# Performance work log

Measured on AMD Instinct MI355X. Metric: run time of the kernel, lower is better.

## Reference

```python
import jax, jax.numpy as jnp
import numpy as np

H = 128          # GRU hidden size (fixed in module)
EPS = 1e-8       # torch CosineSimilarity eps


def _gru_dir(x, w_ih, w_hh, b_ih, b_hh, reverse):
    # x: [B, L, D]; torch GRU gate math, single direction
    B = x.shape[0]
    gx = jnp.einsum('bld,gd->blg', x, w_ih) + b_ih  # [B, L, 3H]

    def step(h, gx_t):
        gh = h @ w_hh.T + b_hh
        xr, xz, xn = jnp.split(gx_t, 3, axis=-1)
        hr, hz, hn = jnp.split(gh, 3, axis=-1)
        r = jax.nn.sigmoid(xr + hr)
        z = jax.nn.sigmoid(xz + hz)
        n = jnp.tanh(xn + r * hn)
        h_new = (1.0 - z) * n + z * h
        return h_new, h_new

    h0 = jnp.zeros((B, H), x.dtype)
    h_last, outs = jax.lax.scan(step, h0, jnp.swapaxes(gx, 0, 1), reverse=reverse)
    return jnp.swapaxes(outs, 0, 1), h_last  # [B, L, H], [B, H]


def _bigru(x, p):
    # p = (w_ih_f, w_hh_f, b_ih_f, b_hh_f, w_ih_b, w_hh_b, b_ih_b, b_hh_b)
    of, hf = _gru_dir(x, p[0], p[1], p[2], p[3], False)
    ob, hb = _gru_dir(x, p[4], p[5], p[6], p[7], True)
    # outs concat = torch bidirectional output; [hf, hb] concat == h_n.transpose(1,0).reshape(B,-1)
    return jnp.concatenate([of, ob], axis=-1), jnp.concatenate([hf, hb], axis=-1)


def _cosnorm(x):
    return x / jnp.maximum(jnp.linalg.norm(x, axis=-1, keepdims=True), EPS)


def _forward(context, options, rnn_p, attn_p):
    ctx_outs, ctx_h = _bigru(context, rnn_p)  # [B, L1, 2H], [B, 2H]

    def per_option(option):  # option: [B, L2, D]
        opt_outs, _ = _bigru(option, rnn_p)  # [B, L2, 2H]
        # cosine-similarity attention == matmul of L2-normalized vectors
        # (replaces the original O(B*L2*L1*2H) repeated tensors, same math)
        att = jnp.einsum('bqh,bkh->bqk', _cosnorm(opt_outs), _cosnorm(ctx_outs))  # [B, L2, L1]
        att = jax.nn.softmax(att, axis=2)  # softmax over context positions (dim=2)
        att_opt = jnp.einsum('bqk,bkh->bqh', att, ctx_outs)  # bmm -> [B, L2, 2H]
        cat = jnp.concatenate([att_opt, opt_outs], axis=-1)  # [B, L2, 4H]
        _, ao_h = _bigru(cat, attn_p)  # [B, 2H]
        num = jnp.sum(ctx_h * ao_h, axis=-1)
        den = jnp.maximum(jnp.linalg.norm(ctx_h, axis=-1), EPS) * \
              jnp.maximum(jnp.linalg.norm(ao_h, axis=-1), EPS)
        return num / den  # [B]

    logits = jax.vmap(per_option)(jnp.swapaxes(options, 0, 1))  # [N, B]
    return jax.nn.softmax(logits.T, axis=1)  # [B, N]


def setup_inputs():
    key = jax.random.key(0)
    ks = jax.random.split(key, 24)
    B, L1, L2, N, D = 64, 512, 50, 10, 300
    inp = {
        'context': jax.random.normal(ks[0], (B, L1, D), jnp.float32),
        'context_lens': jax.random.randint(ks[1], (B,), 1, L1),
        'options': jax.random.normal(ks[2], (B, N, L2, D), jnp.float32),
        'option_lens': jax.random.randint(ks[3], (B, N), 1, L2),
    }
    names = ['rw_ih_f', 'rw_hh_f', 'rb_ih_f', 'rb_hh_f',
             'rw_ih_b', 'rw_hh_b', 'rb_ih_b', 'rb_hh_b',
             'aw_ih_f', 'aw_hh_f', 'ab_ih_f', 'ab_hh_f',
             'aw_ih_b', 'aw_hh_b', 'ab_ih_b', 'ab_hh_b']
    shapes = [(3 * H, D), (3 * H, H), (3 * H,), (3 * H,)] * 2 + \
             [(3 * H, 4 * H), (3 * H, H), (3 * H,), (3 * H,)] * 2
    for i, (n, sh) in enumerate(zip(names, shapes)):
        inp[n] = jax.random.normal(ks[4 + i], sh, jnp.float32) * 0.05
    return inp


def reference(context, context_lens, options, option_lens,
              rw_ih_f, rw_hh_f, rb_ih_f, rb_hh_f,
              rw_ih_b, rw_hh_b, rb_ih_b, rb_hh_b,
              aw_ih_f, aw_hh_f, ab_ih_f, ab_hh_f,
              aw_ih_b, aw_hh_b, ab_ih_b, ab_hh_b):
    rnn_p = (rw_ih_f, rw_hh_f, rb_ih_f, rb_hh_f, rw_ih_b, rw_hh_b, rb_ih_b, rb_hh_b)
    attn_p = (aw_ih_f, aw_hh_f, ab_ih_f, ab_hh_f, aw_ih_b, aw_hh_b, ab_ih_b, ab_hh_b)
    return _forward(context, options, rnn_p, attn_p)
```

## Files before the change

kernel.cpp:

```cpp
#include <hip/hip_runtime.h>
#include <math.h>

#define EPS 1e-8f

typedef _Float16 h2_t __attribute__((ext_vector_type(2)));
typedef _Float16 half8 __attribute__((ext_vector_type(8)));
typedef float f32x4 __attribute__((ext_vector_type(4)));

__device__ __forceinline__ float fsig(float x)  { return 1.0f / (1.0f + __expf(-x)); }
__device__ __forceinline__ float ftanh(float x) { return 1.0f - 2.0f / (1.0f + __expf(2.0f * x)); }

__device__ __forceinline__ void gload16(const _Float16* g, _Float16* lds) {
    __builtin_amdgcn_global_load_lds(
        (const __attribute__((address_space(1))) void*)g,
        (__attribute__((address_space(3))) void*)lds, 16, 0, 0);
}

__device__ __forceinline__ float qsum4(float x) {
    int y1 = __builtin_amdgcn_update_dpp(
        0, __builtin_bit_cast(int, x), 0xB1, 0xF, 0xF, true);
    float s1 = x + __builtin_bit_cast(float, y1);
    int y2 = __builtin_amdgcn_update_dpp(
        0, __builtin_bit_cast(int, s1), 0x4E, 0xF, 0xF, true);
    return s1 + __builtin_bit_cast(float, y2);
}

__global__ __launch_bounds__(256) void prep_w_k(
    const float* __restrict__ rwf, const float* __restrict__ rwb,
    const float* __restrict__ awf, const float* __restrict__ awb,
    const float* __restrict__ rbf, const float* __restrict__ rbb,
    const float* __restrict__ abf, const float* __restrict__ abb,
    const float* __restrict__ rhf, const float* __restrict__ rhb,
    const float* __restrict__ ahf, const float* __restrict__ ahb,
    _Float16* __restrict__ wrh, _Float16* __restrict__ wah,
    _Float16* __restrict__ wr16, _Float16* __restrict__ wa16,
    float* __restrict__ br, float* __restrict__ ba)
{
    int idx = blockIdx.x * 256 + threadIdx.x;
    if (idx < 768 * 320) {
        int g = idx / 320, k = idx % 320;
        float v = 0.f;
        if (k < 300) v = (g < 384) ? rwf[g * 300 + k] : rwb[(g - 384) * 300 + k];
        wrh[idx] = (_Float16)v;
    }
    if (idx < 768 * 512) {
        int g = idx / 512, k = idx % 512;
        wah[idx] = (_Float16)((g < 384) ? awf[g * 512 + k] : awb[(g - 384) * 512 + k]);
    }
    if (idx < 2 * 384 * 128) {
        int d = idx / 49152, r = idx % 49152;
        wr16[idx] = (_Float16)(d ? rhb[r] : rhf[r]);
        wa16[idx] = (_Float16)(d ? ahb[r] : ahf[r]);
    }
    if (idx < 768) {
        br[idx] = (idx < 384) ? rbf[idx] : rbb[idx - 384];
        ba[idx] = (idx < 384) ? abf[idx] : abb[idx - 384];
    }
}

__global__ __launch_bounds__(256) void conv_k(
    const float* __restrict__ ctx, const float* __restrict__ opt,
    _Float16* __restrict__ ctxh, _Float16* __restrict__ opth)
{
    int idx = blockIdx.x * 256 + threadIdx.x;
    if (idx < 32768 * 320) {
        int r = idx / 320, k = idx % 320;
        ctxh[idx] = (k < 300) ? (_Float16)ctx[r * 300 + k] : (_Float16)0.f;
    }
    if (idx < 32000 * 320) {
        int r = idx / 320, k = idx % 320;
        opth[idx] = (k < 300) ? (_Float16)opt[r * 300 + k] : (_Float16)0.f;
    }
}

template <bool TRBS, bool SPLITA, bool HASBIAS, bool DIRECT>
__global__ __launch_bounds__(256, 4) void hgemm_k(
    const _Float16* __restrict__ A, const _Float16* __restrict__ A2,
    const _Float16* __restrict__ B, const float* __restrict__ bias,
    _Float16* __restrict__ C, int M, int N, int K,
    int lda, int ldb, int ldc, long sA, long sB, int bdiv, long sC)
{
    static_assert(!(DIRECT && TRBS), "DIRECT requires NT B layout");
    const int jn = blockIdx.x * 64;
    const int im = blockIdx.y * 64;
    const int z  = blockIdx.z;
    const _Float16* Bb = B + (size_t)(z / bdiv) * sB;
    _Float16* Cb = C + (size_t)z * sC;

    __shared__ __align__(16) _Float16 As[64 * 64];
    __shared__ __align__(16) _Float16 Bs[64 * 64];

    const int tid  = threadIdx.x;
    const int arow = tid >> 2;
    const int akof = (tid & 3) * 8;
    const int lane = tid & 63;
    const int wv   = tid >> 6;
    const int wm   = (wv & 1) * 32;
    const int wn   = (wv >> 1) * 32;
    const int fm   = lane & 15;
    const int quad = lane >> 4;

    f32x4 acc[2][2];
#pragma unroll
    for (int a = 0; a < 2; a++)
#pragma unroll
        for (int b = 0; b < 2; b++) acc[a][b] = (f32x4)0.f;

    for (int k0 = 0; k0 < K; k0 += 64) {
        if constexpr (DIRECT) {
            const int r8 = lane >> 3;
            const int kg = k0 + (lane & 7) * 8;
#pragma unroll
            for (int hh = 0; hh < 2; hh++) {
                const int rb = 8 * (wv + 4 * hh);
                const _Float16* gA;
                if constexpr (SPLITA) {
                    const _Float16* Ah  = A  + (size_t)z * sA;
                    const _Float16* A2h = A2 + (size_t)z * sA;
                    gA = (kg < 256)
                        ? (Ah  + (size_t)(im + rb + r8) * lda + kg)
                        : (A2h + (size_t)(im + rb + r8) * lda + (kg - 256));
                } else {
                    gA = A + (size_t)z * sA + (size_t)(im + rb + r8) * lda + kg;
                }
                gload16(gA, &As[rb * 64]);
                gload16(Bb + (size_t)(jn + rb + r8) * ldb + kg, &Bs[rb * 64]);
            }
        } else {
            {
                const int row = im + arow;
#pragma unroll
                for (int hh = 0; hh < 2; hh++) {
                    half8 av = (half8)(_Float16)0.f;
                    const int kg = k0 + akof + 32 * hh;
                    if (row < M) {
                        if constexpr (SPLITA) {
                            const _Float16* Ah  = A + (size_t)z * sA;
                            const _Float16* A2h = A2 + (size_t)z * sA;
                            const _Float16* ap = (kg < 256)
                                ? (Ah + (size_t)row * lda + kg)
                                : (A2h + (size_t)row * lda + (kg - 256));
                            av = *(const half8*)ap;
                        } else {
                            av = *(const half8*)(A + (size_t)z * sA + (size_t)row * lda + kg);
                        }
                    }
                    *(half8*)&As[arow * 64 + akof + 32 * hh] = av;
                }
            }
            if constexpr (!TRBS) {
#pragma unroll
                for (int hh = 0; hh < 2; hh++) {
                    half8 bv = *(const half8*)(Bb + (size_t)(jn + arow) * ldb
                                               + k0 + akof + 32 * hh);
                    *(half8*)&Bs[arow * 64 + akof + 32 * hh] = bv;
                }
            } else {
                const int kk = tid >> 3, noff = (tid & 7) * 8;
                half8 bv0 = *(const half8*)(Bb + (size_t)(k0 + kk) * ldb + jn + noff);
                half8 bv1 = *(const half8*)(Bb + (size_t)(k0 + kk + 32) * ldb + jn + noff);
#pragma unroll
                for (int e = 0; e < 8; e++) {
                    Bs[(noff + e) * 64 + kk]      = bv0[e];
                    Bs[(noff + e) * 64 + kk + 32] = bv1[e];
                }
            }
        }
        __syncthreads();

        const _Float16* Asp = As + (wm + fm) * 64 + quad * 8;
        const _Float16* Bsp = Bs + (wn + fm) * 64 + quad * 8;
#pragma unroll
        for (int kh = 0; kh < 64; kh += 32) {
            half8 a0 = *(const half8*)(Asp + kh);
            half8 a1 = *(const half8*)(Asp + 16 * 64 + kh);
            half8 b0 = *(const half8*)(Bsp + kh);
            half8 b1 = *(const half8*)(Bsp + 16 * 64 + kh);
            acc[0][0] = __builtin_amdgcn_mfma_f32_16x16x32_f16(a0, b0, acc[0][0], 0, 0, 0);
            acc[0][1] = __builtin_amdgcn_mfma_f32_16x16x32_f16(a0, b1, acc[0][1], 0, 0, 0);
            acc[1][0] = __builtin_amdgcn_mfma_f32_16x16x32_f16(a1, b0, acc[1][0], 0, 0, 0);
            acc[1][1] = __builtin_amdgcn_mfma_f32_16x16x32_f16(a1, b1, acc[1][1], 0, 0, 0);
        }
        __syncthreads();
    }

#pragma unroll
    for (int tm = 0; tm < 2; tm++) {
#pragma unroll
        for (int tn = 0; tn < 2; tn++) {
            const int col  = jn + wn + tn * 16 + fm;
            const int row0 = im + wm + tm * 16 + quad * 4;
            const float bv = HASBIAS ? bias[col] : 0.f;
#pragma unroll
            for (int r = 0; r < 4; r++) {
                const int row = row0 + r;
                if (DIRECT || row < M)
                    Cb[(size_t)row * ldc + col] = (_Float16)(acc[tm][tn][r] + bv);
            }
        }
    }
}

template <int TCMAX>
__global__ __launch_bounds__(512, 2) void gru_rec_k(
    const _Float16* __restrict__ gx,
    const _Float16* __restrict__ whh16,
    const float* __restrict__ bhh_f, const float* __restrict__ bhh_b,
    _Float16* __restrict__ outs_h, float* __restrict__ hfin, int L)
{
    const int dir = blockIdx.x & 1;
    const int s   = blockIdx.x >> 1;
    const int t   = threadIdx.x;
    const int w   = t >> 6;
    const int l   = t & 63;
    const int i   = w * 16 + (l >> 2);
    const int kq  = l & 3;
    const _Float16* Wd = whh16 + (size_t)dir * 49152;
    const float* bh = dir ? bhh_b : bhh_f;

    h2_t w2[3][16];
#pragma unroll
    for (int j = 0; j < 3; j++) {
        const _Float16* Wr = Wd + (size_t)(i + 128 * j) * 128 + 32 * kq;
#pragma unroll
        for (int q = 0; q < 16; q++)
            w2[j][q] = *(const h2_t*)(Wr + 2 * q);
    }
    const float b0 = bh[i], b1 = bh[i + 128], b2 = bh[i + 256];

    __shared__ __align__(16) _Float16 h1[2][128];
    __shared__ __align__(16) _Float16 gxs[TCMAX][384];
    __shared__ __align__(16) _Float16 outb[TCMAX][128];
    if (t < 128) h1[0][t] = (_Float16)0.f;
    float hprev = 0.f;

    constexpr int NST = (TCMAX * 48 + 511) / 512;
    constexpr int NFL = (TCMAX * 16 + 511) / 512;

    for (int t0 = 0; t0 < L; t0 += TCMAX) {
        const int Tc = (L - t0 < TCMAX) ? (L - t0) : TCMAX;
#pragma unroll
        for (int r = 0; r < NST; r++) {
            const int q = t + 512 * r;
            if (q < Tc * 48) {
                const int j = q / 48, off = (q % 48) * 8;
                const int tt = dir ? (L - 1 - (t0 + j)) : (t0 + j);
                *(half8*)&gxs[j][off] =
                    *(const half8*)(gx + ((size_t)s * L + tt) * 768 + dir * 384 + off);
            }
        }
        __syncthreads();

        for (int j = 0; j < Tc; j++) {
            const int cb = (t0 + j) & 1;
            const float xc0 = (float)gxs[j][i];
            const float xc1 = (float)gxs[j][i + 128];
            const float xc2 = (float)gxs[j][i + 256];
            const h2_t* hp = (const h2_t*)&h1[cb][32 * kq];
            float a0 = 0.f, a1 = 0.f, a2 = 0.f;
#pragma unroll
            for (int q = 0; q < 16; q++) {
                h2_t hq = hp[q];
                a0 = __builtin_amdgcn_fdot2(w2[0][q], hq, a0, false);
                a1 = __builtin_amdgcn_fdot2(w2[1][q], hq, a1, false);
                a2 = __builtin_amdgcn_fdot2(w2[2][q], hq, a2, false);
            }
            a0 = qsum4(a0);
            a1 = qsum4(a1);
            a2 = qsum4(a2);
            const float r  = fsig(xc0 + a0 + b0);
            const float zz = fsig(xc1 + a1 + b1);
            const float n  = ftanh(xc2 + r * (a2 + b2));
            const float hnew = (1.0f - zz) * n + zz * hprev;
            hprev = hnew;
            if (kq == 0) {
                h1[cb ^ 1][i] = (_Float16)hnew;
                outb[j][i]    = (_Float16)hnew;
            }
            __syncthreads();
        }

        if (outs_h) {
#pragma unroll
            for (int r = 0; r < NFL; r++) {
                const int q = t + 512 * r;
                if (q < Tc * 16) {
                    const int j = q / 16, off = (q % 16) * 8;
                    const int tt = dir ? (L - 1 - (t0 + j)) : (t0 + j);
                    *(half8*)(outs_h + ((size_t)s * L + tt) * 256 + dir * 128 + off) =
                        *(const half8*)&outb[j][off];
                }
            }
        }
    }
    if (hfin && kq == 0) hfin[(size_t)s * 256 + dir * 128 + i] = hprev;
}

__global__ __launch_bounds__(256) void rowinv_k(const _Float16* __restrict__ x,
                                                float* __restrict__ rinv)
{
    const int row = blockIdx.x;
    float v = (float)x[(size_t)row * 256 + threadIdx.x];
    float ss = v * v;
#pragma unroll
    for (int o = 32; o > 0; o >>= 1) ss += __shfl_down(ss, o);
    __shared__ float ps[4];
    if ((threadIdx.x & 63) == 0) ps[threadIdx.x >> 6] = ss;
    __syncthreads();
    if (threadIdx.x == 0)
        rinv[row] = 1.0f / fmaxf(sqrtf(ps[0] + ps[1] + ps[2] + ps[3]), EPS);
}

__global__ __launch_bounds__(256) void att_softmax_k(
    _Float16* __restrict__ att, const float* __restrict__ rinv_opt_l,
    const float* __restrict__ rinv_ctx, int sbase)
{
    const int row = blockIdx.x;
    const int b = (sbase + row / 50) / 10;
    _Float16* p = att + (size_t)row * 512;
    const float* rc = rinv_ctx + b * 512;
    const float sA = rinv_opt_l[row];
    const int t = threadIdx.x;

    float v0 = (float)p[t]       * (sA * rc[t]);
    float v1 = (float)p[t + 256] * (sA * rc[t + 256]);

    __shared__ float red[4];
    float m = fmaxf(v0, v1);
#pragma unroll
    for (int o = 32; o > 0; o >>= 1) m = fmaxf(m, __shfl_down(m, o));
    if ((t & 63) == 0) red[t >> 6] = m;
    __syncthreads();
    m = fmaxf(fmaxf(red[0], red[1]), fmaxf(red[2], red[3]));
    float e0 = __expf(v0 - m), e1 = __expf(v1 - m);
    float ssum = e0 + e1;
#pragma unroll
    for (int o = 32; o > 0; o >>= 1) ssum += __shfl_down(ssum, o);
    __syncthreads();
    if ((t & 63) == 0) red[t >> 6] = ssum;
    __syncthreads();
    float inv = 1.0f / (red[0] + red[1] + red[2] + red[3]);
    p[t]       = (_Float16)(e0 * inv);
    p[t + 256] = (_Float16)(e1 * inv);
}

__global__ __launch_bounds__(256) void logits_k(const float* __restrict__ ch,
                                                const float* __restrict__ ah,
                                                float* __restrict__ logits)
{
    const int s = blockIdx.x;
    const int b = s / 10;
    const int t = threadIdx.x;
    float a = ch[b * 256 + t];
    float c = ah[(size_t)s * 256 + t];
    float num = a * c, na = a * a, nc = c * c;
#pragma unroll
    for (int o = 32; o > 0; o >>= 1) {
        num += __shfl_down(num, o);
        na  += __shfl_down(na,  o);
        nc  += __shfl_down(nc,  o);
    }
    __shared__ float pn[4], pa[4], pc[4];
    if ((t & 63) == 0) { pn[t >> 6] = num; pa[t >> 6] = na; pc[t >> 6] = nc; }
    __syncthreads();
    if (t == 0) {
        float sn = pn[0] + pn[1] + pn[2] + pn[3];
        float sa = pa[0] + pa[1] + pa[2] + pa[3];
        float sc = pc[0] + pc[1] + pc[2] + pc[3];
        logits[s] = sn / (fmaxf(sqrtf(sa), EPS) * fmaxf(sqrtf(sc), EPS));
    }
}

__global__ __launch_bounds__(64) void soft10_k(const float* __restrict__ logits,
                                               float* __restrict__ out)
{
    const int b = blockIdx.x;
    const int t = threadIdx.x;
    __shared__ float v[10];
    if (t < 10) v[t] = logits[b * 10 + t];
    __syncthreads();
    if (t < 10) {
        float m = v[0];
#pragma unroll
        for (int i = 1; i < 10; i++) m = fmaxf(m, v[i]);
        float ssum = 0.f;
#pragma unroll
        for (int i = 0; i < 10; i++) ssum += __expf(v[i] - m);
        out[b * 10 + t] = __expf(v[t] - m) / ssum;
    }
}

extern "C" void kernel_launch(void* const* d_in, const int* in_sizes, int n_in,
                              void* d_out, int out_size, void* d_ws, size_t ws_size,
                              hipStream_t stream)
{
    const float* context = (const float*)d_in[0];
    const float* options = (const float*)d_in[2];
    const float* rw_ih_f = (const float*)d_in[4];
    const float* rw_hh_f = (const float*)d_in[5];
    const float* rb_ih_f = (const float*)d_in[6];
    const float* rb_hh_f = (const float*)d_in[7];
    const float* rw_ih_b = (const float*)d_in[8];
    const float* rw_hh_b = (const float*)d_in[9];
    const float* rb_ih_b = (const float*)d_in[10];
    const float* rb_hh_b = (const float*)d_in[11];
    const float* aw_ih_f = (const float*)d_in[12];
    const float* aw_hh_f = (const float*)d_in[13];
    const float* ab_ih_f = (const float*)d_in[14];
    const float* ab_hh_f = (const float*)d_in[15];
    const float* aw_ih_b = (const float*)d_in[16];
    const float* aw_hh_b = (const float*)d_in[17];
    const float* ab_ih_b = (const float*)d_in[18];
    const float* ab_hh_b = (const float*)d_in[19];

    const size_t persist = 15222144;
    static const int cands[6][2] = {{1,2},{1,4},{2,4},{2,8},{4,16},{8,16}};
    int CC = 8, OC = 16;
    for (int idx = 0; idx < 6; idx++) {
        size_t bc_ = 64 / cands[idx][0], sc_ = 640 / cands[idx][1];
        size_t p = bc_ * 196608;
        if (sc_ * 32000 > p) p = sc_ * 32000;
        if ((persist + p + 2 * sc_ * 6400) * 4 <= ws_size) {
            CC = cands[idx][0]; OC = cands[idx][1]; break;
        }
    }
    const int bc = 64 / CC;
    const int sc = 640 / OC;
    size_t poolsz = (size_t)bc * 196608;
    if ((size_t)sc * 32000 > poolsz) poolsz = (size_t)sc * 32000;

    float* ws = (float*)d_ws;
    size_t off = 0;
    _Float16* wrh   = (_Float16*)(ws + off); off += 122880;
    float*    br    = ws + off;              off += 768;
    _Float16* wah   = (_Float16*)(ws + off); off += 196608;
    float*    ba    = ws + off;              off += 768;
    _Float16* wr16  = (_Float16*)(ws + off); off += 49152;
    _Float16* wa16  = (_Float16*)(ws + off); off += 49152;
    _Float16* couts = (_Float16*)(ws + off); off += 4194304;
    float*    ctxhf = ws + off;              off += 16384;
    float*    aohf  = ws + off;              off += 163840;
    float*    logits= ws + off;              off += 640;
    float*    rinvc = ws + off;              off += 32768;
    float*    rinvo = ws + off;              off += 32000;
    _Float16* ctxh  = (_Float16*)(ws + off); off += 5242880;
    _Float16* opth  = (_Float16*)(ws + off); off += 5120000;
    _Float16* POOL  = (_Float16*)(ws + off); off += poolsz;
    _Float16* P2H   = (_Float16*)(ws + off); off += (size_t)sc * 6400;
    _Float16* P3H   = (_Float16*)(ws + off); off += (size_t)sc * 6400;
    _Float16* ATT   = POOL + (size_t)sc * 38400;

    prep_w_k<<<1536, 256, 0, stream>>>(rw_ih_f, rw_ih_b, aw_ih_f, aw_ih_b,
                                       rb_ih_f, rb_ih_b, ab_ih_f, ab_ih_b,
                                       rw_hh_f, rw_hh_b, aw_hh_f, aw_hh_b,
                                       wrh, wah, wr16, wa16, br, ba);
    conv_k<<<40960, 256, 0, stream>>>(context, options, ctxh, opth);

    for (int c = 0; c < CC; c++) {
        const int Mc = bc * 512;
        hgemm_k<false, false, true, true><<<dim3(12, Mc / 64, 1), 256, 0, stream>>>(
            ctxh + (size_t)c * Mc * 320, nullptr, wrh, br, POOL,
            Mc, 768, 320, 320, 320, 768, 0, 0, 1, 0);
        gru_rec_k<64><<<2 * bc, 512, 0, stream>>>(
            POOL, wr16, rb_hh_f, rb_hh_b,
            couts + (size_t)c * Mc * 256, ctxhf + (size_t)c * bc * 256, 512);
    }

    rowinv_k<<<32768, 256, 0, stream>>>(couts, rinvc);

    for (int o = 0; o < OC; o++) {
        const int base = o * sc;
        const int Mo = sc * 50;
        const bool modir = (Mo % 64) == 0;
        const _Float16* ctxB = couts + (size_t)(base / 10) * 131072;

        if (modir)
            hgemm_k<false, false, true, true><<<dim3(12, Mo / 64, 1), 256, 0, stream>>>(
                opth + (size_t)base * 50 * 320, nullptr, wrh, br, POOL,
                Mo, 768, 320, 320, 320, 768, 0, 0, 1, 0);
        else
            hgemm_k<false, false, true, false><<<dim3(12, (Mo + 63) / 64, 1), 256, 0, stream>>>(
                opth + (size_t)base * 50 * 320, nullptr, wrh, br, POOL,
                Mo, 768, 320, 320, 320, 768, 0, 0, 1, 0);
        gru_rec_k<50><<<2 * sc, 512, 0, stream>>>(
            POOL, wr16, rb_hh_f, rb_hh_b, P2H, nullptr, 50);
        rowinv_k<<<Mo, 256, 0, stream>>>(P2H, rinvo + (size_t)base * 50);
        hgemm_k<false, false, false, false><<<dim3(8, 1, sc), 256, 0, stream>>>(
            P2H, nullptr, ctxB, nullptr, ATT,
            50, 512, 256, 256, 256, 512, 12800, 131072, 10, 25600);
        att_softmax_k<<<Mo, 256, 0, stream>>>(ATT, rinvo + (size_t)base * 50,
                                              rinvc, base);
        hgemm_k<true, false, false, false><<<dim3(4, 1, sc), 256, 0, stream>>>(
            ATT, nullptr, ctxB, nullptr, P3H,
            50, 256, 512, 512, 256, 256, 25600, 131072, 10, 12800);
        if (modir)
            hgemm_k<false, true, true, true><<<dim3(12, Mo / 64, 1), 256, 0, stream>>>(
                P3H, P2H, wah, ba, POOL,
                Mo, 768, 512, 256, 512, 768, 0, 0, 1, 0);
        else
            hgemm_k<false, true, true, false><<<dim3(12, (Mo + 63) / 64, 1), 256, 0, stream>>>(
                P3H, P2H, wah, ba, POOL,
                Mo, 768, 512, 256, 512, 768, 0, 0, 1, 0);
        gru_rec_k<50><<<2 * sc, 512, 0, stream>>>(
            POOL, wa16, ab_hh_f, ab_hh_b, nullptr, aohf + (size_t)base * 256, 50);
    }

    logits_k<<<640, 256, 0, stream>>>(ctxhf, aohf, logits);
    soft10_k<<<64, 64, 0, stream>>>(logits, (float*)d_out);
}
```

Baseline: 1.078 ms.

## Add 128-row GEMM tile, vectorize conversion and row-norm kernels, reorder GRU loads

Adds a 128x64-tile GEMM variant for the input-projection GEMMs, used when M is a multiple of 128. Each block now covers twice as many rows, so the shared B tile is reused more and fewer blocks are launched. The fp32-to-fp16 conversion kernel becomes a grid-stride loop that writes 8 halves per thread, and the row-norm kernel uses one wavefront with vector loads. The GRU step now reads its input gates after the dot products, which may hide LDS latency. The larger tile doubles the A tile in LDS and the accumulator count per thread, which may reduce occupancy.

Measured after the change: 1.038 ms. 3.7% less time.

```diff
diff --git a/kernel.cpp b/kernel.cpp
--- a/kernel.cpp
+++ b/kernel.cpp
@@ -62,14 +62,33 @@
     const float* __restrict__ ctx, const float* __restrict__ opt,
     _Float16* __restrict__ ctxh, _Float16* __restrict__ opth)
 {
-    int idx = blockIdx.x * 256 + threadIdx.x;
-    if (idx < 32768 * 320) {
-        int r = idx / 320, k = idx % 320;
-        ctxh[idx] = (k < 300) ? (_Float16)ctx[r * 300 + k] : (_Float16)0.f;
-    }
-    if (idx < 32000 * 320) {
-        int r = idx / 320, k = idx % 320;
-        opth[idx] = (k < 300) ? (_Float16)opt[r * 300 + k] : (_Float16)0.f;
+    const long NCTX = 32768L * 40;
+    const long NTOT = NCTX + 32000L * 40;
+    for (long c = (long)blockIdx.x * 256 + threadIdx.x; c < NTOT;
+         c += (long)gridDim.x * 256) {
+        const bool isctx = c < NCTX;
+        const long cc = isctx ? c : c - NCTX;
+        const int r  = (int)(cc / 40);
+        const int k0 = (int)(cc % 40) * 8;
+        const float* src = (isctx ? ctx : opt) + (size_t)r * 300;
+        _Float16*    dst = (isctx ? ctxh : opth) + (size_t)r * 320 + k0;
+        half8 hv;
+        if (k0 + 8 <= 300) {
+            f32x4 f0 = *(const f32x4*)(src + k0);
+            f32x4 f1 = *(const f32x4*)(src + k0 + 4);
+#pragma unroll
+            for (int e = 0; e < 4; e++) {
+                hv[e]     = (_Float16)f0[e];
+                hv[e + 4] = (_Float16)f1[e];
+            }
+        } else {
+#pragma unroll
+            for (int e = 0; e < 8; e++) {
+                const int k = k0 + e;
+                hv[e] = (k < 300) ? (_Float16)src[k] : (_Float16)0.f;
+            }
+        }
+        *(half8*)dst = hv;
     }
 }
 
@@ -201,6 +220,98 @@
     }
 }
 
+template <bool SPLITA, bool HASBIAS>
+__global__ __launch_bounds__(256, 4) void hgemm2_k(
+    const _Float16* __restrict__ A, const _Float16* __restrict__ A2,
+    const _Float16* __restrict__ B, const float* __restrict__ bias,
+    _Float16* __restrict__ C, int M, int N, int K,
+    int lda, int ldb, int ldc, long sA, long sB, int bdiv, long sC)
+{
+    const int jn = blockIdx.x * 64;
+    const int im = blockIdx.y * 128;
+    const int z  = blockIdx.z;
+    const _Float16* Bb = B + (size_t)(z / bdiv) * sB;
+    _Float16* Cb = C + (size_t)z * sC;
+
+    __shared__ __align__(16) _Float16 As[128 * 64];
+    __shared__ __align__(16) _Float16 Bs[64 * 64];
+
+    const int tid  = threadIdx.x;
+    const int lane = tid & 63;
+    const int wv   = tid >> 6;
+    const int wm   = (wv & 1) * 32;
+    const int wn   = (wv >> 1) * 32;
+    const int fm   = lane & 15;
+    const int quad = lane >> 4;
+
+    f32x4 acc[2][2][2];
+#pragma unroll
+    for (int m = 0; m < 2; m++)
+#pragma unroll
+        for (int a = 0; a < 2; a++)
+#pragma unroll
+            for (int b = 0; b < 2; b++) acc[m][a][b] = (f32x4)0.f;
+
+    for (int k0 = 0; k0 < K; k0 += 64) {
+        const int r8 = lane >> 3;
+        const int kg = k0 + (lane & 7) * 8;
+#pragma unroll
+        for (int hh = 0; hh < 4; hh++) {
+            const int rb = 8 * (wv + 4 * hh);
+            const _Float16* gA;
+            if constexpr (SPLITA) {
+                const _Float16* Ah  = A  + (size_t)z * sA;
+                const _Float16* A2h = A2 + (size_t)z * sA;
+                gA = (kg < 256)
+                    ? (Ah  + (size_t)(im + rb + r8) * lda + kg)
+                    : (A2h + (size_t)(im + rb + r8) * lda + (kg - 256));
+            } else {
+                gA = A + (size_t)z * sA + (size_t)(im + rb + r8) * lda + kg;
+            }
+            gload16(gA, &As[rb * 64]);
+        }
+#pragma unroll
+        for (int hh = 0; hh < 2; hh++) {
+            const int rb = 8 * (wv + 4 * hh);
+            gload16(Bb + (size_t)(jn + rb + r8) * ldb + kg, &Bs[rb * 64]);
+        }
+        __syncthreads();
+
+        const _Float16* Bsp = Bs + (wn + fm) * 64 + quad * 8;
+#pragma unroll
+        for (int kh = 0; kh < 64; kh += 32) {
+            half8 b0 = *(const half8*)(Bsp + kh);
+            half8 b1 = *(const half8*)(Bsp + 16 * 64 + kh);
+#pragma unroll
+            for (int mh = 0; mh < 2; mh++) {
+                const _Float16* Asp = As + (mh * 64 + wm + fm) * 64 + quad * 8;
+                half8 a0 = *(const half8*)(Asp + kh);
+                half8 a1 = *(const half8*)(Asp + 16 * 64 + kh);
+                acc[mh][0][0] = __builtin_amdgcn_mfma_f32_16x16x32_f16(a0, b0, acc[mh][0][0], 0, 0, 0);
+                acc[mh][0][1] = __builtin_amdgcn_mfma_f32_16x16x32_f16(a0, b1, acc[mh][0][1], 0, 0, 0);
+                acc[mh][1][0] = __builtin_amdgcn_mfma_f32_16x16x32_f16(a1, b0, acc[mh][1][0], 0, 0, 0);
+                acc[mh][1][1] = __builtin_amdgcn_mfma_f32_16x16x32_f16(a1, b1, acc[mh][1][1], 0, 0, 0);
+            }
+        }
+        __syncthreads();
+    }
+
+#pragma unroll
+    for (int mh = 0; mh < 2; mh++)
+#pragma unroll
+        for (int tm = 0; tm < 2; tm++)
+#pragma unroll
+            for (int tn = 0; tn < 2; tn++) {
+                const int col  = jn + wn + tn * 16 + fm;
+                const int row0 = im + mh * 64 + wm + tm * 16 + quad * 4;
+                const float bv = HASBIAS ? bias[col] : 0.f;
+#pragma unroll
+                for (int r = 0; r < 4; r++)
+                    Cb[(size_t)(row0 + r) * ldc + col] =
+                        (_Float16)(acc[mh][tm][tn][r] + bv);
+            }
+}
+
 template <int TCMAX>
 __global__ __launch_bounds__(512, 2) void gru_rec_k(
     const _Float16* __restrict__ gx,
@@ -253,9 +364,6 @@
 
         for (int j = 0; j < Tc; j++) {
             const int cb = (t0 + j) & 1;
-            const float xc0 = (float)gxs[j][i];
-            const float xc1 = (float)gxs[j][i + 128];
-            const float xc2 = (float)gxs[j][i + 256];
             const h2_t* hp = (const h2_t*)&h1[cb][32 * kq];
             float a0 = 0.f, a1 = 0.f, a2 = 0.f;
 #pragma unroll
@@ -268,6 +376,9 @@
             a0 = qsum4(a0);
             a1 = qsum4(a1);
             a2 = qsum4(a2);
+            const float xc0 = (float)gxs[j][i];
+            const float xc1 = (float)gxs[j][i + 128];
+            const float xc2 = (float)gxs[j][i + 256];
             const float r  = fsig(xc0 + a0 + b0);
             const float zz = fsig(xc1 + a1 + b1);
             const float n  = ftanh(xc2 + r * (a2 + b2));
@@ -296,19 +407,19 @@
     if (hfin && kq == 0) hfin[(size_t)s * 256 + dir * 128 + i] = hprev;
 }
 
-__global__ __launch_bounds__(256) void rowinv_k(const _Float16* __restrict__ x,
-                                                float* __restrict__ rinv)
+__global__ __launch_bounds__(64) void rowinv_k(const _Float16* __restrict__ x,
+                                               float* __restrict__ rinv)
 {
     const int row = blockIdx.x;
-    float v = (float)x[(size_t)row * 256 + threadIdx.x];
-    float ss = v * v;
+    const _Float16* p = x + (size_t)row * 256 + threadIdx.x * 4;
+    const h2_t v0 = *(const h2_t*)p;
+    const h2_t v1 = *(const h2_t*)(p + 2);
+    float ss = (float)v0[0] * (float)v0[0] + (float)v0[1] * (float)v0[1]
+             + (float)v1[0] * (float)v1[0] + (float)v1[1] * (float)v1[1];
 #pragma unroll
     for (int o = 32; o > 0; o >>= 1) ss += __shfl_down(ss, o);
-    __shared__ float ps[4];
-    if ((threadIdx.x & 63) == 0) ps[threadIdx.x >> 6] = ss;
-    __syncthreads();
     if (threadIdx.x == 0)
-        rinv[row] = 1.0f / fmaxf(sqrtf(ps[0] + ps[1] + ps[2] + ps[3]), EPS);
+        rinv[row] = 1.0f / fmaxf(sqrtf(ss), EPS);
 }
 
 __global__ __launch_bounds__(256) void att_softmax_k(
@@ -454,11 +565,11 @@
                                        rb_ih_f, rb_ih_b, ab_ih_f, ab_ih_b,
                                        rw_hh_f, rw_hh_b, aw_hh_f, aw_hh_b,
                                        wrh, wah, wr16, wa16, br, ba);
-    conv_k<<<40960, 256, 0, stream>>>(context, options, ctxh, opth);
+    conv_k<<<4096, 256, 0, stream>>>(context, options, ctxh, opth);
 
     for (int c = 0; c < CC; c++) {
         const int Mc = bc * 512;
-        hgemm_k<false, false, true, true><<<dim3(12, Mc / 64, 1), 256, 0, stream>>>(
+        hgemm2_k<false, true><<<dim3(12, Mc / 128, 1), 256, 0, stream>>>(
             ctxh + (size_t)c * Mc * 320, nullptr, wrh, br, POOL,
             Mc, 768, 320, 320, 320, 768, 0, 0, 1, 0);
         gru_rec_k<64><<<2 * bc, 512, 0, stream>>>(
@@ -466,15 +577,18 @@
             couts + (size_t)c * Mc * 256, ctxhf + (size_t)c * bc * 256, 512);
     }
 
-    rowinv_k<<<32768, 256, 0, stream>>>(couts, rinvc);
+    rowinv_k<<<32768, 64, 0, stream>>>(couts, rinvc);
 
     for (int o = 0; o < OC; o++) {
         const int base = o * sc;
         const int Mo = sc * 50;
-        const bool modir = (Mo % 64) == 0;
         const _Float16* ctxB = couts + (size_t)(base / 10) * 131072;
 
-        if (modir)
+        if ((Mo % 128) == 0)
+            hgemm2_k<false, true><<<dim3(12, Mo / 128, 1), 256, 0, stream>>>(
+                opth + (size_t)base * 50 * 320, nullptr, wrh, br, POOL,
+                Mo, 768, 320, 320, 320, 768, 0, 0, 1, 0);
+        else if ((Mo % 64) == 0)
             hgemm_k<false, false, true, true><<<dim3(12, Mo / 64, 1), 256, 0, stream>>>(
                 opth + (size_t)base * 50 * 320, nullptr, wrh, br, POOL,
                 Mo, 768, 320, 320, 320, 768, 0, 0, 1, 0);
@@ -484,7 +598,7 @@
                 Mo, 768, 320, 320, 320, 768, 0, 0, 1, 0);
         gru_rec_k<50><<<2 * sc, 512, 0, stream>>>(
             POOL, wr16, rb_hh_f, rb_hh_b, P2H, nullptr, 50);
-        rowinv_k<<<Mo, 256, 0, stream>>>(P2H, rinvo + (size_t)base * 50);
+        rowinv_k<<<Mo, 64, 0, stream>>>(P2H, rinvo + (size_t)base * 50);
         hgemm_k<false, false, false, false><<<dim3(8, 1, sc), 256, 0, stream>>>(
             P2H, nullptr, ctxB, nullptr, ATT,
             50, 512, 256, 256, 256, 512, 12800, 131072, 10, 25600);
@@ -493,7 +607,11 @@
         hgemm_k<true, false, false, false><<<dim3(4, 1, sc), 256, 0, stream>>>(
             ATT, nullptr, ctxB, nullptr, P3H,
             50, 256, 512, 512, 256, 256, 25600, 131072, 10, 12800);
-        if (modir)
+        if ((Mo % 128) == 0)
+            hgemm2_k<true, true><<<dim3(12, Mo / 128, 1), 256, 0, stream>>>(
+                P3H, P2H, wah, ba, POOL,
+                Mo, 768, 512, 256, 512, 768, 0, 0, 1, 0);
+        else if ((Mo % 64) == 0)
             hgemm_k<false, true, true, true><<<dim3(12, Mo / 64, 1), 256, 0, stream>>>(
                 P3H, P2H, wah, ba, POOL,
                 Mo, 768, 512, 256, 512, 768, 0, 0, 1, 0);
```
